# Kernel optimization log

Measured on AMD Instinct MI355X. Metric: run time of the kernel, lower is better.

## Reference

```python
import jax, jax.numpy as jnp
import numpy as np

N_SRC = 100_000   # hetero[s].num_nodes
N_DST = 100_000   # hetero[d].num_nodes
E     = 800_000   # edge_index.size(1)
D_SRC = 256       # node_dims['src']
D_DST = 256       # node_dims['dst']
D_REL = 128       # d_rel


def setup_inputs() -> dict:
    key = jax.random.key(0)
    ks = jax.random.split(key, 6)
    x_src = jax.random.normal(ks[0], (N_SRC, D_SRC), jnp.float32)
    x_dst = jax.random.normal(ks[1], (N_DST, D_DST), jnp.float32)
    # nn.Linear(d_in, d_rel, bias=False) weights, stored transposed as [d_in, d_rel]
    W_src = jax.random.normal(ks[2], (D_SRC, D_REL), jnp.float32) / np.sqrt(D_SRC).astype(np.float32)
    W_dst = jax.random.normal(ks[3], (D_DST, D_REL), jnp.float32) / np.sqrt(D_DST).astype(np.float32)
    edge_src = jax.random.randint(ks[4], (E,), 0, N_SRC, jnp.int32)  # edge_index[0]
    edge_dst = jax.random.randint(ks[5], (E,), 0, N_DST, jnp.int32)  # edge_index[1]
    return {"x_src": x_src, "x_dst": x_dst, "W_src": W_src, "W_dst": W_dst,
            "edge_src": edge_src, "edge_dst": edge_dst}


def reference(x_src, x_dst, W_src, W_dst, edge_src, edge_dst):
    # Per-type linear projection (bias-free), as in self.proj[nt](feats)
    p_src = x_src @ W_src            # [N_src, d_rel]
    p_dst = x_dst @ W_dst            # projected per module, unused by this edge type
    del p_dst

    # Degree of each destination (A.sum(dim=1)), clamped to >= 1.
    deg = jax.ops.segment_sum(jnp.ones((E,), jnp.float32), edge_dst,
                              num_segments=N_DST)
    deg = jnp.maximum(deg, 1.0)      # [N_dst]

    # Degree-normalized SpMM: sum of source features per destination / deg.
    # (coalescing duplicate edges sums their unit values; segment_sum matches.)
    agg = jax.ops.segment_sum(p_src[edge_src], edge_dst,
                              num_segments=N_DST)            # [N_dst, d_rel]
    dst = agg / deg[:, None]

    # rel_embs[et] = {'dst': dst, 'src_in': x_proj[s], 'deg_dst': deg}
    return dst, p_src, deg
```

## Files before the change

### kernel.cpp

```cpp
#include <hip/hip_runtime.h>
#include <hip/hip_bf16.h>

#define D_SRC 256
#define D_REL 128

typedef __bf16 bf16x8 __attribute__((ext_vector_type(8)));
typedef float f32x4 __attribute__((ext_vector_type(4)));
typedef float f32x2 __attribute__((ext_vector_type(2)));

typedef const __attribute__((address_space(1))) void GASV;
typedef __attribute__((address_space(3))) void LASV;

__global__ __launch_bounds__(64) void prep_w_kernel(const float* __restrict__ W,
                                                    bf16x8* __restrict__ Wt) {
    int c = blockIdx.x;
    int ks = c >> 3, n = c & 7;
    int lane = threadIdx.x;
    int col = n * 16 + (lane & 15);
    int k0 = ks * 32 + (lane >> 4) * 8;
    bf16x8 v;
#pragma unroll
    for (int j = 0; j < 8; ++j) v[j] = (__bf16)W[(size_t)(k0 + j) * D_REL + col];
    Wt[c * 64 + lane] = v;
}

__global__ __launch_bounds__(256, 4) void proj_gemm_kernel(
    const float* __restrict__ x, const f32x4* __restrict__ Wt,
    unsigned short* __restrict__ out_bf, int M) {
    __shared__ float xlds[32 * 256];
    int tid = threadIdx.x;
    int wid = tid >> 6, lane = tid & 63;
    int r = lane & 15, kq = lane >> 4;
    int row0 = blockIdx.x * 32;

#pragma unroll
    for (int j = 0; j < 8; ++j) {
        int rl = wid * 8 + j;
        int grow = min(row0 + rl, M - 1);
        const float* src = x + (size_t)grow * D_SRC + ((lane ^ j) << 2);
        __builtin_amdgcn_global_load_lds((GASV*)src, (LASV*)&xlds[rl * 256], 16, 0, 0);
    }

    f32x4 wfv[2][8];
#pragma unroll
    for (int s = 0; s < 2; ++s)
#pragma unroll
        for (int ks = 0; ks < 8; ++ks)
            wfv[s][ks] = Wt[(ks * 8 + wid * 2 + s) * 64 + lane];
#pragma unroll
    for (int s = 0; s < 2; ++s)
#pragma unroll
        for (int ks = 0; ks < 8; ++ks)
            asm volatile("" : "+v"(wfv[s][ks]));

    __syncthreads();

    f32x4 acc[2][2];
#pragma unroll
    for (int t = 0; t < 2; ++t)
#pragma unroll
        for (int s = 0; s < 2; ++s) acc[t][s] = (f32x4)(0.f);

    const f32x4* xl = (const f32x4*)xlds;
    int r8 = r & 7;
#pragma unroll
    for (int ks = 0; ks < 8; ++ks) {
        int q0 = ks * 8 + kq * 2;
#pragma unroll
        for (int t = 0; t < 2; ++t) {
            int rl = t * 16 + r;
            f32x4 a0 = xl[rl * 64 + (q0 ^ r8)];
            f32x4 a1 = xl[rl * 64 + ((q0 + 1) ^ r8)];
            bf16x8 xf;
            xf[0] = (__bf16)a0[0]; xf[1] = (__bf16)a0[1];
            xf[2] = (__bf16)a0[2]; xf[3] = (__bf16)a0[3];
            xf[4] = (__bf16)a1[0]; xf[5] = (__bf16)a1[1];
            xf[6] = (__bf16)a1[2]; xf[7] = (__bf16)a1[3];
            acc[t][0] = __builtin_amdgcn_mfma_f32_16x16x32_bf16(
                __builtin_bit_cast(bf16x8, wfv[0][ks]), xf, acc[t][0], 0, 0, 0);
            acc[t][1] = __builtin_amdgcn_mfma_f32_16x16x32_bf16(
                __builtin_bit_cast(bf16x8, wfv[1][ks]), xf, acc[t][1], 0, 0, 0);
        }
    }

    int col0 = wid * 32;
#pragma unroll
    for (int t = 0; t < 2; ++t) {
        int prow = row0 + t * 16 + r;
        if (prow < M) {
            size_t o0 = (size_t)prow * D_REL + col0 + kq * 4;
            ushort4 b0, b1;
            b0.x = __bfloat16_as_ushort(__float2bfloat16(acc[t][0][0]));
            b0.y = __bfloat16_as_ushort(__float2bfloat16(acc[t][0][1]));
            b0.z = __bfloat16_as_ushort(__float2bfloat16(acc[t][0][2]));
            b0.w = __bfloat16_as_ushort(__float2bfloat16(acc[t][0][3]));
            b1.x = __bfloat16_as_ushort(__float2bfloat16(acc[t][1][0]));
            b1.y = __bfloat16_as_ushort(__float2bfloat16(acc[t][1][1]));
            b1.z = __bfloat16_as_ushort(__float2bfloat16(acc[t][1][2]));
            b1.w = __bfloat16_as_ushort(__float2bfloat16(acc[t][1][3]));
            *(ushort4*)(out_bf + o0) = b0;
            *(ushort4*)(out_bf + o0 + 16) = b1;
        }
    }
}

__global__ __launch_bounds__(256) void convert_kernel(
    const uint4* __restrict__ p_bf, float* __restrict__ out, int n8) {
    int i = blockIdx.x * 256 + threadIdx.x;
    if (i >= n8) return;
    uint4 v = p_bf[i];
    f32x4 lo, hi;
    lo[0] = __uint_as_float(v.x << 16);
    lo[1] = __uint_as_float(v.x & 0xffff0000u);
    lo[2] = __uint_as_float(v.y << 16);
    lo[3] = __uint_as_float(v.y & 0xffff0000u);
    hi[0] = __uint_as_float(v.z << 16);
    hi[1] = __uint_as_float(v.z & 0xffff0000u);
    hi[2] = __uint_as_float(v.w << 16);
    hi[3] = __uint_as_float(v.w & 0xffff0000u);
    f32x4* o = (f32x4*)(out + (size_t)i * 8);
    __builtin_nontemporal_store(lo, o);
    __builtin_nontemporal_store(hi, o + 1);
}

__global__ void count_kernel(const int* __restrict__ edge_dst, int* __restrict__ deg_i,
                             int* __restrict__ pos_arr, int E) {
    int e = blockIdx.x * 256 + threadIdx.x;
    if (e < E) pos_arr[e] = atomicAdd(&deg_i[edge_dst[e]], 1);
}

__global__ __launch_bounds__(1024) void scan_blocks(
    const int* __restrict__ deg_i, int* __restrict__ incl,
    int* __restrict__ bsums, int n) {
    int i = blockIdx.x * 1024 + threadIdx.x;
    int v = (i < n) ? deg_i[i] : 0;
    int lane = threadIdx.x & 63;
    int wid = threadIdx.x >> 6;
    int x = v;
#pragma unroll
    for (int off = 1; off < 64; off <<= 1) {
        int y = __shfl_up(x, off, 64);
        if (lane >= off) x += y;
    }
    __shared__ int wsum[16];
    if (lane == 63) wsum[wid] = x;
    __syncthreads();
    if (wid == 0 && lane < 16) {
        int s = wsum[lane];
#pragma unroll
        for (int off = 1; off < 16; off <<= 1) {
            int y = __shfl_up(s, off, 64);
            if (lane >= off) s += y;
        }
        wsum[lane] = s;
    }
    __syncthreads();
    int add = (wid > 0) ? wsum[wid - 1] : 0;
    x += add;
    if (i < n) incl[i] = x;
    if (threadIdx.x == 1023) bsums[blockIdx.x] = x;
}

__global__ __launch_bounds__(128) void scan_sums(int* __restrict__ bs, int nb) {
    __shared__ int tmp[128];
    int t = threadIdx.x;
    int v = (t < nb) ? bs[t] : 0;
    tmp[t] = v;
    __syncthreads();
    for (int off = 1; off < 128; off <<= 1) {
        int y = 0;
        if (t >= off) y = tmp[t - off];
        __syncthreads();
        tmp[t] += y;
        __syncthreads();
    }
    if (t < nb) bs[t] = tmp[t] - v;
}

__global__ __launch_bounds__(1024) void finalize_kernel(
    const int* __restrict__ deg_i, const int* __restrict__ incl,
    const int* __restrict__ bsums, int* __restrict__ row_start,
    float* __restrict__ deg_out, int n, int E) {
    int i = blockIdx.x * 1024 + threadIdx.x;
    if (i < n) {
        int off = bsums[blockIdx.x];
        row_start[i] = off + incl[i] - deg_i[i];
        deg_out[i] = (float)max(deg_i[i], 1);
    }
    if (i == 0) row_start[n] = E;
}

__global__ void fill_kernel(const int* __restrict__ edge_src,
                            const int* __restrict__ edge_dst,
                            const int* __restrict__ row_start,
                            const int* __restrict__ pos_arr,
                            int* __restrict__ bucket, int E) {
    int e = blockIdx.x * 256 + threadIdx.x;
    if (e < E) {
        int d = edge_dst[e];
        bucket[row_start[d] + pos_arr[e]] = edge_src[e];
    }
}

__global__ __launch_bounds__(256) void gather_kernel(
    const unsigned int* __restrict__ p_bf, const int* __restrict__ row_start,
    const int* __restrict__ bucket, const float* __restrict__ deg_out,
    float* __restrict__ dst, int n) {
    int row = blockIdx.x * 4 + (threadIdx.x >> 6);
    int lane = threadIdx.x & 63;
    if (row >= n) return;
    int beg = row_start[row], end = row_start[row + 1];
    float ax = 0.f, ay = 0.f;
    int idx = beg;
    for (; idx + 8 <= end; idx += 8) {
        int s[8];
        unsigned int v[8];
#pragma unroll
        for (int u = 0; u < 8; ++u) s[u] = bucket[idx + u];
#pragma unroll
        for (int u = 0; u < 8; ++u) v[u] = p_bf[(size_t)s[u] * 64 + lane];
#pragma unroll
        for (int u = 0; u < 8; ++u) {
            ax += __uint_as_float(v[u] << 16);
            ay += __uint_as_float(v[u] & 0xffff0000u);
        }
    }
    for (; idx + 4 <= end; idx += 4) {
        int s0 = bucket[idx + 0], s1 = bucket[idx + 1];
        int s2 = bucket[idx + 2], s3 = bucket[idx + 3];
        unsigned int v0 = p_bf[(size_t)s0 * 64 + lane];
        unsigned int v1 = p_bf[(size_t)s1 * 64 + lane];
        unsigned int v2 = p_bf[(size_t)s2 * 64 + lane];
        unsigned int v3 = p_bf[(size_t)s3 * 64 + lane];
        ax += __uint_as_float(v0 << 16) + __uint_as_float(v1 << 16)
            + __uint_as_float(v2 << 16) + __uint_as_float(v3 << 16);
        ay += __uint_as_float(v0 & 0xffff0000u) + __uint_as_float(v1 & 0xffff0000u)
            + __uint_as_float(v2 & 0xffff0000u) + __uint_as_float(v3 & 0xffff0000u);
    }
    for (; idx < end; ++idx) {
        int s = bucket[idx];
        unsigned int v = p_bf[(size_t)s * 64 + lane];
        ax += __uint_as_float(v << 16);
        ay += __uint_as_float(v & 0xffff0000u);
    }
    float dinv = 1.0f / deg_out[row];
    f32x2 o;
    o[0] = ax * dinv;
    o[1] = ay * dinv;
    f32x2* dp = (f32x2*)dst + (size_t)row * 64 + lane;
    __builtin_nontemporal_store(o, dp);
}

extern "C" void kernel_launch(void* const* d_in, const int* in_sizes, int n_in,
                              void* d_out, int out_size, void* d_ws, size_t ws_size,
                              hipStream_t stream) {
    const float* x_src = (const float*)d_in[0];
    const float* W_src = (const float*)d_in[2];
    const int* edge_src = (const int*)d_in[4];
    const int* edge_dst = (const int*)d_in[5];

    const int N_SRC = in_sizes[0] / D_SRC;
    const int N_DST = in_sizes[1] / D_SRC;
    const int E = in_sizes[4];

    float* out_dst = (float*)d_out;
    float* out_psrc = out_dst + (size_t)N_DST * D_REL;
    float* out_deg = out_psrc + (size_t)N_SRC * D_REL;

    int* deg_i = (int*)d_ws;
    int* incl = deg_i + N_DST;
    int* row_start = incl + N_DST;
    int* bsums = row_start + N_DST + 1;
    int* pos_arr = bsums + 128;
    int* bucket = pos_arr + E;
    size_t int_bytes = (size_t)(3 * N_DST + 1 + 128 + 2 * (size_t)E) * sizeof(int);
    size_t wt_off = (int_bytes + 255) & ~(size_t)255;
    bf16x8* Wt = (bf16x8*)((char*)d_ws + wt_off);
    size_t pbf_off = wt_off + 65536;
    unsigned short* p_bf = (unsigned short*)((char*)d_ws + pbf_off);

    (void)hipMemsetAsync(deg_i, 0, (size_t)N_DST * sizeof(int), stream);
    prep_w_kernel<<<64, 64, 0, stream>>>(W_src, Wt);
    proj_gemm_kernel<<<(N_SRC + 31) / 32, 256, 0, stream>>>(
        x_src, (const f32x4*)Wt, p_bf, N_SRC);
    {
        int n8 = N_SRC * D_REL / 8;
        convert_kernel<<<(n8 + 255) / 256, 256, 0, stream>>>(
            (const uint4*)p_bf, out_psrc, n8);
    }
    count_kernel<<<(E + 255) / 256, 256, 0, stream>>>(edge_dst, deg_i, pos_arr, E);
    int nb = (N_DST + 1023) / 1024;
    scan_blocks<<<nb, 1024, 0, stream>>>(deg_i, incl, bsums, N_DST);
    scan_sums<<<1, 128, 0, stream>>>(bsums, nb);
    finalize_kernel<<<nb, 1024, 0, stream>>>(deg_i, incl, bsums, row_start, out_deg, N_DST, E);
    fill_kernel<<<(E + 255) / 256, 256, 0, stream>>>(edge_src, edge_dst, row_start, pos_arr, bucket, E);
    gather_kernel<<<(N_DST + 3) / 4, 256, 0, stream>>>(
        (const unsigned int*)p_bf, row_start, bucket, out_deg, out_dst, N_DST);
}
```

Before: 151.0 us.

## Fuse degree count into projection GEMM and drop convert and scan_sums kernels

Folds the memset of the degree array into prep_w_kernel and merges the edge-count atomics into the projection GEMM launch as extra blocks, so both run concurrently. The GEMM now writes the fp32 p_src output directly instead of running a separate bf16-to-fp32 convert pass. The scan_sums kernel is removed, and each finalize block computes its own prefix of the block sums with a wave reduction. This cuts the number of launches and one full read/write pass over p_src. In exchange, the GEMM writes extra fp32 data, and the output p_src is no longer bf16-rounded, which changes its numerics slightly (it becomes more accurate).

```diff
diff --git a/kernel.cpp b/kernel.cpp
--- a/kernel.cpp
+++ b/kernel.cpp
@@ -12,7 +12,8 @@
 typedef __attribute__((address_space(3))) void LASV;
 
 __global__ __launch_bounds__(64) void prep_w_kernel(const float* __restrict__ W,
-                                                    bf16x8* __restrict__ Wt) {
+                                                    bf16x8* __restrict__ Wt,
+                                                    int* __restrict__ deg_i, int ndeg) {
     int c = blockIdx.x;
     int ks = c >> 3, n = c & 7;
     int lane = threadIdx.x;
@@ -22,13 +23,25 @@
 #pragma unroll
     for (int j = 0; j < 8; ++j) v[j] = (__bf16)W[(size_t)(k0 + j) * D_REL + col];
     Wt[c * 64 + lane] = v;
-}
-
-__global__ __launch_bounds__(256, 4) void proj_gemm_kernel(
+    for (int i = blockIdx.x * 64 + lane; i < ndeg; i += 64 * 64) deg_i[i] = 0;
+}
+
+__global__ __launch_bounds__(256, 4) void proj_count_kernel(
     const float* __restrict__ x, const f32x4* __restrict__ Wt,
-    unsigned short* __restrict__ out_bf, int M) {
+    float* __restrict__ out_f32, unsigned short* __restrict__ out_bf, int M,
+    const int* __restrict__ edge_dst, int* __restrict__ deg_i,
+    int* __restrict__ pos_arr, int E, int nproj, int ncb) {
     __shared__ float xlds[32 * 256];
     int tid = threadIdx.x;
+
+    if (blockIdx.x >= nproj) {
+        int cb = blockIdx.x - nproj;
+        int stride = ncb * 256;
+        for (int e = cb * 256 + tid; e < E; e += stride)
+            pos_arr[e] = atomicAdd(&deg_i[edge_dst[e]], 1);
+        return;
+    }
+
     int wid = tid >> 6, lane = tid & 63;
     int r = lane & 15, kq = lane >> 4;
     int row0 = blockIdx.x * 32;
@@ -89,6 +102,8 @@
         int prow = row0 + t * 16 + r;
         if (prow < M) {
             size_t o0 = (size_t)prow * D_REL + col0 + kq * 4;
+            __builtin_nontemporal_store(acc[t][0], (f32x4*)(out_f32 + o0));
+            __builtin_nontemporal_store(acc[t][1], (f32x4*)(out_f32 + o0 + 16));
             ushort4 b0, b1;
             b0.x = __bfloat16_as_ushort(__float2bfloat16(acc[t][0][0]));
             b0.y = __bfloat16_as_ushort(__float2bfloat16(acc[t][0][1]));
@@ -104,31 +119,6 @@
     }
 }
 
-__global__ __launch_bounds__(256) void convert_kernel(
-    const uint4* __restrict__ p_bf, float* __restrict__ out, int n8) {
-    int i = blockIdx.x * 256 + threadIdx.x;
-    if (i >= n8) return;
-    uint4 v = p_bf[i];
-    f32x4 lo, hi;
-    lo[0] = __uint_as_float(v.x << 16);
-    lo[1] = __uint_as_float(v.x & 0xffff0000u);
-    lo[2] = __uint_as_float(v.y << 16);
-    lo[3] = __uint_as_float(v.y & 0xffff0000u);
-    hi[0] = __uint_as_float(v.z << 16);
-    hi[1] = __uint_as_float(v.z & 0xffff0000u);
-    hi[2] = __uint_as_float(v.w << 16);
-    hi[3] = __uint_as_float(v.w & 0xffff0000u);
-    f32x4* o = (f32x4*)(out + (size_t)i * 8);
-    __builtin_nontemporal_store(lo, o);
-    __builtin_nontemporal_store(hi, o + 1);
-}
-
-__global__ void count_kernel(const int* __restrict__ edge_dst, int* __restrict__ deg_i,
-                             int* __restrict__ pos_arr, int E) {
-    int e = blockIdx.x * 256 + threadIdx.x;
-    if (e < E) pos_arr[e] = atomicAdd(&deg_i[edge_dst[e]], 1);
-}
-
 __global__ __launch_bounds__(1024) void scan_blocks(
     const int* __restrict__ deg_i, int* __restrict__ incl,
     int* __restrict__ bsums, int n) {
@@ -161,29 +151,24 @@
     if (threadIdx.x == 1023) bsums[blockIdx.x] = x;
 }
 
-__global__ __launch_bounds__(128) void scan_sums(int* __restrict__ bs, int nb) {
-    __shared__ int tmp[128];
-    int t = threadIdx.x;
-    int v = (t < nb) ? bs[t] : 0;
-    tmp[t] = v;
-    __syncthreads();
-    for (int off = 1; off < 128; off <<= 1) {
-        int y = 0;
-        if (t >= off) y = tmp[t - off];
-        __syncthreads();
-        tmp[t] += y;
-        __syncthreads();
-    }
-    if (t < nb) bs[t] = tmp[t] - v;
-}
-
 __global__ __launch_bounds__(1024) void finalize_kernel(
     const int* __restrict__ deg_i, const int* __restrict__ incl,
     const int* __restrict__ bsums, int* __restrict__ row_start,
     float* __restrict__ deg_out, int n, int E) {
-    int i = blockIdx.x * 1024 + threadIdx.x;
+    __shared__ int soff;
+    int bid = blockIdx.x;
+    if (threadIdx.x < 64) {
+        int lane = threadIdx.x;
+        int s = 0;
+        for (int i = lane; i < bid; i += 64) s += bsums[i];
+#pragma unroll
+        for (int m = 32; m >= 1; m >>= 1) s += __shfl_xor(s, m, 64);
+        if (lane == 0) soff = s;
+    }
+    __syncthreads();
+    int off = soff;
+    int i = bid * 1024 + threadIdx.x;
     if (i < n) {
-        int off = bsums[blockIdx.x];
         row_start[i] = off + incl[i] - deg_i[i];
         deg_out[i] = (float)max(deg_i[i], 1);
     }
@@ -279,19 +264,16 @@
     size_t pbf_off = wt_off + 65536;
     unsigned short* p_bf = (unsigned short*)((char*)d_ws + pbf_off);
 
-    (void)hipMemsetAsync(deg_i, 0, (size_t)N_DST * sizeof(int), stream);
-    prep_w_kernel<<<64, 64, 0, stream>>>(W_src, Wt);
-    proj_gemm_kernel<<<(N_SRC + 31) / 32, 256, 0, stream>>>(
-        x_src, (const f32x4*)Wt, p_bf, N_SRC);
+    prep_w_kernel<<<64, 64, 0, stream>>>(W_src, Wt, deg_i, N_DST);
     {
-        int n8 = N_SRC * D_REL / 8;
-        convert_kernel<<<(n8 + 255) / 256, 256, 0, stream>>>(
-            (const uint4*)p_bf, out_psrc, n8);
-    }
-    count_kernel<<<(E + 255) / 256, 256, 0, stream>>>(edge_dst, deg_i, pos_arr, E);
+        int nproj = (N_SRC + 31) / 32;
+        int ncb = 768;
+        proj_count_kernel<<<nproj + ncb, 256, 0, stream>>>(
+            x_src, (const f32x4*)Wt, out_psrc, p_bf, N_SRC,
+            edge_dst, deg_i, pos_arr, E, nproj, ncb);
+    }
     int nb = (N_DST + 1023) / 1024;
     scan_blocks<<<nb, 1024, 0, stream>>>(deg_i, incl, bsums, N_DST);
-    scan_sums<<<1, 128, 0, stream>>>(bsums, nb);
     finalize_kernel<<<nb, 1024, 0, stream>>>(deg_i, incl, bsums, row_start, out_deg, N_DST, E);
     fill_kernel<<<(E + 255) / 256, 256, 0, stream>>>(edge_src, edge_dst, row_start, pos_arr, bucket, E);
     gather_kernel<<<(N_DST + 3) / 4, 256, 0, stream>>>(
```

After: 134.5 us. 10.9% less time.
